# Performance work log

Hardware: AMD Instinct MI355X
Metric: run time of the kernel (lower is better)

Reference implementation:

```python
import jax, jax.numpy as jnp
import numpy as np

B, HGRID, D_MODEL = 4, 64, 96
D_INNER, D_STATE, DT_RANK, K = 192, 16, 6, 4
L = HGRID * HGRID


def setup_inputs() -> dict:
    key = jax.random.key(0)
    ks = jax.random.split(key, 12)
    C, N, R, D = D_INNER, D_STATE, DT_RANK, D_MODEL
    s = 0.02
    x = jax.random.normal(ks[0], (B, L, D), jnp.float32)
    in_proj_w = jax.random.normal(ks[1], (2 * C, D)) * s
    fft_w1 = jax.random.normal(ks[2], (C, C)) * s
    fft_b1 = jnp.zeros((C,))
    fft_w2 = jax.random.normal(ks[3], (C, C)) * s
    fft_b2 = jnp.zeros((C,))
    wave_w = jax.random.normal(ks[4], (C, C, 3, 3)) * s
    wave_b = jnp.zeros((C,))
    dw_w = jax.random.normal(ks[5], (C, 1, 3, 3)) * 0.1
    dw_b = jnp.zeros((C,))
    sym_w = jnp.asarray(0.3, jnp.float32)
    x_proj_w = jax.random.normal(ks[6], (K, R + 2 * N, C)) * s
    dt_std = R ** -0.5
    dt_w = jax.random.uniform(ks[7], (K, C, R), minval=-dt_std, maxval=dt_std)
    dt = jnp.exp(jax.random.uniform(ks[8], (K, C)) * (np.log(0.1) - np.log(0.001)) + np.log(0.001))
    dt = jnp.maximum(dt, 1e-4)
    dt_b = dt + jnp.log(-jnp.expm1(-dt))  # inverse softplus init as in dt_init
    A_logs = jnp.log(jnp.tile(jnp.arange(1, N + 1, dtype=jnp.float32), (K * C, 1)))  # [K*C, N]
    Ds = jnp.ones((K * C,))
    out_norm_g = jnp.ones((C,))
    out_norm_b = jnp.zeros((C,))
    out_proj_w = jax.random.normal(ks[9], (D, C)) * s
    rms_w = jnp.ones((D,))
    return dict(x=x, in_proj_w=in_proj_w, fft_w1=fft_w1, fft_b1=fft_b1, fft_w2=fft_w2,
                fft_b2=fft_b2, wave_w=wave_w, wave_b=wave_b, dw_w=dw_w, dw_b=dw_b,
                sym_w=sym_w, x_proj_w=x_proj_w, dt_w=dt_w, dt_b=dt_b, A_logs=A_logs,
                Ds=Ds, out_norm_g=out_norm_g, out_norm_b=out_norm_b,
                out_proj_w=out_proj_w, rms_w=rms_w)


def _conv2d(x, w, b, groups=1):
    y = jax.lax.conv_general_dilated(x, w, (1, 1), 'SAME', feature_group_count=groups,
                                     dimension_numbers=('NCHW', 'OIHW', 'NCHW'))
    return y + b[None, :, None, None]


def _haar_dwt(x):
    # orthonormal single-level Haar on 2x2 blocks
    a = x[..., 0::2, 0::2]; b = x[..., 0::2, 1::2]
    c = x[..., 1::2, 0::2]; d = x[..., 1::2, 1::2]
    return ((a + b + c + d) * 0.5, (a - b + c - d) * 0.5,
            (a + b - c - d) * 0.5, (a - b - c + d) * 0.5)


def _haar_idwt(ll, lh, hl, hh):
    a = (ll + lh + hl + hh) * 0.5; b = (ll - lh + hl - hh) * 0.5
    c = (ll + lh - hl - hh) * 0.5; d = (ll - lh - hl + hh) * 0.5
    Bb, Cc, H2, W2 = ll.shape
    top = jnp.stack([a, b], -1).reshape(Bb, Cc, H2, 2 * W2)
    bot = jnp.stack([c, d], -1).reshape(Bb, Cc, H2, 2 * W2)
    return jnp.stack([top, bot], -2).reshape(Bb, Cc, 2 * H2, 2 * W2)


def _freq_model(x, fft_w1, fft_b1, fft_w2, fft_b2, wave_w, wave_b):
    Bb, C, H, W = x.shape
    xf = jnp.fft.rfft2(x, norm='ortho')
    m = jax.nn.gelu(jnp.einsum('bchw,oc->bohw', jnp.abs(xf), fft_w1)
                    + fft_b1[None, :, None, None], approximate=False)
    mag = jnp.einsum('bchw,oc->bohw', m, fft_w2) + fft_b2[None, :, None, None]
    x_fourier = jnp.fft.irfft2(mag * jnp.exp(1j * jnp.angle(xf)), s=(H, W), norm='ortho')
    ll, lh, hl, hh = _haar_dwt(x)
    lh = _conv2d(lh, wave_w, wave_b)
    hl = _conv2d(hl, wave_w, wave_b)
    hh = _conv2d(hh, wave_w, wave_b)
    x_wavelet = _haar_idwt(ll, lh, hl, hh)
    return x + x_fourier + x_wavelet


def _selective_scan(xs, delta, A, Bs, Cs, Ds):
    # xs/delta: [B,K,C,L]; A: [K,C,N]; Bs/Cs: [B,K,N,L]; Ds: [K,C]
    Bb, Kk, C, Ll = xs.shape
    N = A.shape[-1]
    u_t = jnp.moveaxis(xs, -1, 0)     # [L,B,K,C]
    d_t = jnp.moveaxis(delta, -1, 0)
    B_t = jnp.moveaxis(Bs, -1, 0)     # [L,B,K,N]
    C_t = jnp.moveaxis(Cs, -1, 0)

    def step(h, inp):
        u, dd, bb, cc = inp
        h = jnp.exp(dd[..., None] * A) * h + (dd * u)[..., None] * bb[:, :, None, :]
        return h, jnp.einsum('bkcn,bkn->bkc', h, cc)

    h0 = jnp.zeros((Bb, Kk, C, N), xs.dtype)
    _, ys = jax.lax.scan(step, h0, (u_t, d_t, B_t, C_t))
    return jnp.moveaxis(ys, 0, -1) + xs * Ds[None, :, :, None]


def _forward(x, in_proj_w, fft_w1, fft_b1, fft_w2, fft_b2, wave_w, wave_b, dw_w, dw_b,
             sym_w, x_proj_w, dt_w, dt_b, A_logs, Ds, out_norm_g, out_norm_b,
             out_proj_w, rms_w):
    Bb, Ll, D = x.shape
    H = W = HGRID
    C, N, R = D_INNER, D_STATE, DT_RANK
    # RMSNorm (residual pre-norm)
    xn = x * jax.lax.rsqrt(jnp.mean(x * x, -1, keepdims=True) + 1e-5) * rms_w
    xz = xn.reshape(Bb, H, W, D) @ in_proj_w.T            # [B,H,W,2C]
    xi, z = jnp.split(xz, 2, axis=-1)
    xc = jnp.transpose(xi, (0, 3, 1, 2))                  # NCHW
    xc = xc + _freq_model(xc, fft_w1, fft_b1, fft_w2, fft_b2, wave_w, wave_b)
    a = jax.nn.silu(_conv2d(xc, dw_w, dw_b, groups=C))    # depthwise 3x3
    # 4-direction sequences
    x_flat = a.reshape(Bb, C, Ll)
    x_t = jnp.transpose(a, (0, 1, 3, 2)).reshape(Bb, C, Ll)
    xs = jnp.stack([x_flat, x_t, x_flat[..., ::-1], x_t[..., ::-1]], axis=1)  # [B,4,C,L]
    x_dbl = jnp.einsum('bkdl,kcd->bkcl', xs, x_proj_w)
    dts, Bs, Cs = jnp.split(x_dbl, [R, R + N], axis=2)
    dts = jnp.einsum('bkrl,kdr->bkdl', dts, dt_w)
    delta = jax.nn.softplus(dts + dt_b[None, :, :, None])
    A = -jnp.exp(A_logs).reshape(K, C, N)
    out_y = _selective_scan(xs, delta, A, Bs, Cs, Ds.reshape(K, C))  # [B,4,C,L]
    wh = jnp.transpose(out_y[:, 1].reshape(Bb, C, W, H), (0, 1, 3, 2)).reshape(Bb, C, Ll)
    iwh = jnp.transpose(out_y[:, 3, :, ::-1].reshape(Bb, C, W, H), (0, 1, 3, 2)).reshape(Bb, C, Ll)
    y = out_y[:, 0] + out_y[:, 2, :, ::-1] + wh + iwh     # [B,C,L]
    # lightweight symmetry enhancement
    y4 = y.reshape(Bb, C, H, W)
    wgt = jax.nn.sigmoid(sym_w)
    enh = y4 * (1 - wgt) + 0.5 * (y4 + y4[..., ::-1]) * wgt
    yf = y + 0.2 * enh.reshape(Bb, C, Ll)
    yf = jnp.transpose(yf, (0, 2, 1)).reshape(Bb, H, W, C)
    # LayerNorm
    mu = yf.mean(-1, keepdims=True)
    var = ((yf - mu) ** 2).mean(-1, keepdims=True)
    yn = (yf - mu) * jax.lax.rsqrt(var + 1e-5) * out_norm_g + out_norm_b
    out = (yn * jax.nn.silu(z)) @ out_proj_w.T
    return out.reshape(Bb, Ll, D) + x  # residual


def reference(x, in_proj_w, fft_w1, fft_b1, fft_w2, fft_b2, wave_w, wave_b, dw_w, dw_b,
              sym_w, x_proj_w, dt_w, dt_b, A_logs, Ds, out_norm_g, out_norm_b,
              out_proj_w, rms_w):
    return _forward(x, in_proj_w, fft_w1, fft_b1, fft_w2, fft_b2, wave_w, wave_b,
                    dw_w, dw_b, sym_w, x_proj_w, dt_w, dt_b, A_logs, Ds,
                    out_norm_g, out_norm_b, out_proj_w, rms_w)
```

## Files before the change

kernel.cpp:

```cpp
#include <hip/hip_runtime.h>
#include <hip/hip_bf16.h>

#define CI 192
#define LL_ 4096

typedef __bf16 v8bf __attribute__((ext_vector_type(8)));
typedef float  v4f  __attribute__((ext_vector_type(4)));
typedef float  v8f  __attribute__((ext_vector_type(8)));
typedef unsigned short v8us __attribute__((ext_vector_type(8)));

__device__ __forceinline__ unsigned short f2bf(float v){
  unsigned int u = __float_as_uint(v);
  return (unsigned short)((u + 0x7FFFu + ((u >> 16) & 1u)) >> 16);
}

__global__ __launch_bounds__(256) void k_zero(float* __restrict__ p, int n){
  int i = blockIdx.x*256 + threadIdx.x;
  if (i < n) p[i] = 0.f;
}

__global__ __launch_bounds__(256) void k_rms_inproj(const float* __restrict__ x,
    const float* __restrict__ rmsw, const float* __restrict__ ipw,
    float* __restrict__ xc, float* __restrict__ zT){
  int og = blockIdx.x & 7; int lt = (blockIdx.x >> 3) & 63; int b = blockIdx.x >> 9;
// ... 258 lines not shown
  __syncthreads();
  const unsigned short* base = lhT + (size_t)img*196608;
  for (int idx = tid; idx < 3072; idx += 256){
    int r = idx / 768; int t = idx - r*768;
    int pc = t / 24;   int icg = t - pc*24;
    int gr = 2*mt - 1 + r;
    if (gr >= 0 && gr < 32){
      v8us v = *(const v8us*)&base[((size_t)gr*32 + pc)*192 + icg*8];
      int pix = r*34 + 1 + pc;
      *(v8us*)&Aband[pix*192 + ((icg*8) ^ ((pix & 7) << 3))] = v;
    }
  }
  __syncthreads();
  v4f acc[4];
  #pragma unroll
  for (int t2 = 0; t2 < 4; t2++) acc[t2] = (v4f){0.f,0.f,0.f,0.f};
  #pragma unroll
  for (int q = 0; q < 9; q++){
    int ky = q/3, kx = q - ky*3;
    if (q < 8){
      #pragma unroll
      for (int icc = 0; icc < 6; icc++)
        bnxt[icc] = *(const v8us*)&wrow[(size_t)(q+1)*36864 + icc*32];
    }
    #pragma unroll
    for (int icc = 0; icc < 6; icc++){
      int c0 = icc*32;
      v8bf bv = __builtin_bit_cast(v8bf, bcur[icc]);
      #pragma unroll
      for (int t2 = 0; t2 < 4; t2++){
        int mm = t2*16 + n16;
        int pix = ((mm >> 5) + ky)*34 + (mm & 31) + kx;
        const unsigned short* Ap = &Aband[pix*192 + ((c0 + quad*8) ^ ((pix & 7) << 3))];
        v8bf av = __builtin_bit_cast(v8bf, *(const v8us*)Ap);
        acc[t2] = __builtin_amdgcn_mfma_f32_16x16x32_bf16(av, bv, acc[t2], 0, 0, 0);
      }
    }
    #pragma unroll
    for (int icc = 0; icc < 6; icc++) bcur[icc] = bnxt[icc];
  }
  __syncthreads();
  #pragma unroll
  for (int t2 = 0; t2 < 4; t2++)
    #pragma unroll
    for (int r = 0; r < 4; r++)
      T[(16*t2 + quad*4 + r)*65 + 16*wv + n16] = acc[t2][r];
  __syncthreads();
  float* outb = wnew + (size_t)img*196608;
  for (int idx = tid; idx < 4096; idx += 256){
    int mm = idx & 63, oc = idx >> 6;
    outb[(size_t)(o0 + oc)*1024 + mt*64 + mm] = T[mm*65 + oc];
  }
}

__global__ __launch_bounds__(256) void k_ifwd(const float* __restrict__ fre2,
    const float* __restrict__ fim2, const float* __restrict__ xc,
    const float* __restrict__ ll, const float* __restrict__ wnew, const float* __restrict__ wb,
    const float* __restrict__ dww, const float* __restrict__ dwb,
    float* __restrict__ ab, float* __restrict__ aT){
  int plane = blockIdx.x;
  int c = plane % 192;
  __shared__ __align__(16) float sm[13504];
  float* gr  = sm;
  float* gi  = sm + 2304;
  float* ur  = sm + 4608;
  float* ui  = sm + 6912;
  float* sx2 = sm + 9216;
  float* t64r = sm + 13376; float* t64i = sm + 13440;
  float* scratch = sm;
  int tid = threadIdx.x;
  {
    size_t gbase = (size_t)plane*2112;
    for (int idx = tid; idx < 528; idx += 256){
      float4 vr_ = *(const float4*)&fre2[gbase + 4*idx];
      float4 vi_ = *(const float4*)&fim2[gbase + 4*idx];
      #pragma unroll
      for (int e = 0; e < 4; e++){
        int i = 4*idx + e;
        int f = i/33, k = i - f*33;
        float re = (e==0)?vr_.x:((e==1)?vr_.y:((e==2)?vr_.z:vr_.w));
        float im = (e==0)?vi_.x:((e==1)?vi_.y:((e==2)?vi_.z:vi_.w));
        gr[f*36 + k] = re; gi[f*36 + k] = im;
      }
    }
  }
  if (tid < 64){ t64r[tid] = cospif((float)tid/32.0f); t64i[tid] = sinpif((float)tid/32.0f); }
  __syncthreads();
  {
    int hp = tid & 31, g = tid >> 5;
    float stepr = cospif((float)hp/32.0f), stepi = sinpif((float)hp/32.0f);
    v4f a0r = (v4f)0.f, a0i = (v4f)0.f, a1r = (v4f)0.f, a1i = (v4f)0.f;
    float b0r=0.f, b0i=0.f, b1r=0.f, b1i=0.f;
    for (int fb = 0; fb < 4; fb++){
      int m = ((fb*16)*hp) & 63;
      float twr = t64r[m], twi = t64i[m];
      for (int ff = 0; ff < 16; ff++){
        int f = fb*16 + ff;
        float sg = (f & 1) ? -1.f : 1.f;
        v4f Gr = *(const v4f*)&gr[f*36 + 4*g];
        v4f Gi = *(const v4f*)&gi[f*36 + 4*g];
        v4f pr = Gr*twr - Gi*twi;
        v4f pi = Gr*twi + Gi*twr;
        a0r += pr; a0i += pi;
        a1r += sg*pr; a1i += sg*pi;
        if (g == 0){
          float Tr = gr[f*36 + 32], Ti = gi[f*36 + 32];
          float prs = Tr*twr - Ti*twi, pis = Tr*twi + Ti*twr;
          b0r += prs; b0i += pis; b1r += sg*prs; b1i += sg*pis;
        }
        float nr = twr*stepr - twi*stepi, ni = twr*stepi + twi*stepr;
        twr = nr; twi = ni;
      }
    }
    #pragma unroll
    for (int j = 0; j < 4; j++){
      int k = 4*g + j;
      float ck = (k == 0) ? (1.f/64.f) : (2.f/64.f);
      ur[hp*36 + k] = a0r[j]*ck;       ui[hp*36 + k] = a0i[j]*ck;
      ur[(hp+32)*36 + k] = a1r[j]*ck;  ui[(hp+32)*36 + k] = a1i[j]*ck;
    }
    if (g == 0){
      ur[hp*36 + 32] = b0r*(1.f/64.f);      ui[hp*36 + 32] = b0i*(1.f/64.f);
      ur[(hp+32)*36 + 32] = b1r*(1.f/64.f); ui[(hp+32)*36 + 32] = b1i*(1.f/64.f);
    }
  }
  __syncthreads();
  {
    int h = tid & 63, wg = tid >> 6;
    v8f accL = (v8f)0.f, accH = (v8f)0.f, twr, twi, sr, si;
    #pragma unroll
    for (int j = 0; j < 8; j++){
      int wl = 8*wg + j;
      sr[j] = t64r[wl]; si[j] = t64i[wl];
      twr[j] = 1.f; twi[j] = 0.f;
    }
    float acc32 = 0.f;
    for (int kb = 0; kb < 8; kb++){
      v4f U4 = *(const v4f*)&ur[h*36 + 4*kb];
      v4f V4 = *(const v4f*)&ui[h*36 + 4*kb];
      #pragma unroll
      for (int e = 0; e < 4; e++){
        int k = 4*kb + e;
        float Ur = U4[e], Ui = V4[e];
        if (wg == 0) acc32 += (k & 1) ? -Ur : Ur;
        v8f p = Ur*twr, q = Ui*twi;
        accL += p - q;
        accH += p + q;
        v8f nr = twr*sr - twi*si;
        v8f ni = twr*si + twi*sr;
        twr = nr; twi = ni;
      }
    }
    {
      float Ur = ur[h*36 + 32], Ui = ui[h*36 + 32];
      if (wg == 0) acc32 += Ur;
      v8f p = Ur*twr, q = Ui*twi;
      accL += p - q;
      accH += p + q;
    }
    #pragma unroll
    for (int j = 0; j < 8; j++){
      int wl = 8*wg + j;
      sx2[h*65 + wl] = accL[j];
      if (wl == 0) sx2[h*65 + 32] = acc32;
      else         sx2[h*65 + 64 - wl] = accH[j];
    }
  }
  __syncthreads();
  {
    float bia = wb[c];
    #pragma unroll
    for (int it = 0; it < 8; it++){
      int idx = tid + it*256;
      int h = idx >> 5, pw = idx & 31;
      int w0 = pw*2;
      size_t q = (size_t)plane*1024 + (size_t)(h >> 1)*32 + pw;
      float LL = ll[q];
      float LH = wnew[q] + bia;
      float HL = wnew[786432 + q] + bia;
      float HH = wnew[1572864 + q] + bia;
      float2 xc2 = *(const float2*)&xc[(size_t)plane*4096 + h*64 + w0];
      float v0, v1;
      if (!(h & 1)){ v0 = (LL + LH + HL + HH)*0.5f; v1 = (LL - LH + HL - HH)*0.5f; }
      else         { v0 = (LL + LH - HL - HH)*0.5f; v1 = (LL - LH - HL + HH)*0.5f; }
      sx2[h*65 + w0]     += 2.0f*xc2.x + v0;
      sx2[h*65 + w0 + 1] += 2.0f*xc2.y + v1;
    }
  }
  __syncthreads();
  {
    float wk[9];
    #pragma unroll
    for (int q = 0; q < 9; q++) wk[q] = dww[c*9 + q];
    float dbv = dwb[c];
    int w = tid & 63, st = tid >> 6;
    int h0 = st*16;
    bool wl_ok = (w > 0), wr_ok = (w < 63);
    float r0l, r0c, r0r, r1l, r1c, r1r;
    if (h0 > 0){
      r0l = wl_ok ? sx2[(h0-1)*65 + w-1] : 0.f;
      r0c = sx2[(h0-1)*65 + w];
      r0r = wr_ok ? sx2[(h0-1)*65 + w+1] : 0.f;
    } else { r0l = 0.f; r0c = 0.f; r0r = 0.f; }
    r1l = wl_ok ? sx2[h0*65 + w-1] : 0.f;
    r1c = sx2[h0*65 + w];
    r1r = wr_ok ? sx2[h0*65 + w+1] : 0.f;
    #pragma unroll
    for (int hh2 = 0; hh2 < 16; hh2++){
      int h = h0 + hh2;
      float r2l, r2c, r2r;
      if (h < 63){
        r2l = wl_ok ? sx2[(h+1)*65 + w-1] : 0.f;
        r2c = sx2[(h+1)*65 + w];
        r2r = wr_ok ? sx2[(h+1)*65 + w+1] : 0.f;
      } else { r2l = 0.f; r2c = 0.f; r2r = 0.f; }
      float acc = dbv + r0l*wk[0] + r0c*wk[1] + r0r*wk[2]
                      + r1l*wk[3] + r1c*wk[4] + r1r*wk[5]
                      + r2l*wk[6] + r2c*wk[7] + r2r*wk[8];
      scratch[h*65 + w] = acc / (1.f + __expf(-acc));
      r0l = r1l; r0c = r1c; r0r = r1r;
      r1l = r2l; r1c = r2c; r1r = r2r;
    }
  }
  __syncthreads();
  float* abp = ab + (size_t)plane*4096;
  float* aTp = aT + (size_t)plane*4096;
  for (int p = tid; p < 4096; p += 256){
    abp[p] = scratch[(p >> 6)*65 + (p & 63)];
    aTp[p] = scratch[(p & 63)*65 + (p >> 6)];
  }
}

__global__ __launch_bounds__(256) void k_xproj(const float* __restrict__ ab,
    const float* __restrict__ aT, const float* __restrict__ xpw,
    float* __restrict__ Bsb, float* __restrict__ Csb, float* __restrict__ dlsb,
    float* __restrict__ xsb){
  int bid = blockIdx.x;
  int s = bid & 63; int k = (bid >> 6) & 3; int b = bid >> 8;
  int tid = threadIdx.x;
  __shared__ float als[96][65];
  __shared__ float dls[6][64];
  int l0 = s << 6;
  const float* src = (k & 1) ? aT : ab;
  bool rev = (k >= 2);
  int i = tid & 63, wg = tid >> 6;
  const float* wr[10];
  #pragma unroll
  for (int r = 0; r < 10; r++){
    int cp = wg + 4*r; if (cp > 37) cp = 37;
    int off = __builtin_amdgcn_readfirstlane((k*38 + cp)*192);
    wr[r] = xpw + off;
  }
  float acc[10];
  #pragma unroll
  for (int r = 0; r < 10; r++) acc[r] = 0.f;
  size_t xbase = ((size_t)(b*4 + k)*4096 + l0)*192;
  #pragma unroll
  for (int half = 0; half < 2; half++){
    int d0 = half*96;
    for (int idx = tid; idx < 1536; idx += 256){
      int d = idx >> 4, i4 = idx & 15;
      const float* rowp = src + ((size_t)b*192 + d0 + d)*4096;
      if (!rev){
        float4 v = *(const float4*)&rowp[l0 + 4*i4];
        als[d][4*i4+0] = v.x; als[d][4*i4+1] = v.y;
        als[d][4*i4+2] = v.z; als[d][4*i4+3] = v.w;
      } else {
        float4 v = *(const float4*)&rowp[4092 - l0 - 4*i4];
        als[d][4*i4+0] = v.w; als[d][4*i4+1] = v.z;
        als[d][4*i4+2] = v.y; als[d][4*i4+3] = v.x;
      }
    }
    __syncthreads();
    for (int d = 0; d < 96; d++){
      float v = als[d][i];
      #pragma unroll
      for (int r = 0; r < 10; r++) acc[r] += v*wr[r][d0 + d];
    }
    for (int idx = tid; idx < 1536; idx += 256){
      int ii = idx / 24, cc = (idx - (idx/24)*24)*4;
      float4 v;
      v.x = als[cc+0][ii]; v.y = als[cc+1][ii];
      v.z = als[cc+2][ii]; v.w = als[cc+3][ii];
      *(float4*)&xsb[xbase + (size_t)ii*192 + d0 + cc] = v;
    }
    __syncthreads();
  }
  #pragma unroll
  for (int r = 0; r < 10; r++){
    int cp = wg + 4*r;
    if (cp > 37) continue;
    if (cp < 6) dls[cp][i] = acc[r];
    else if (cp < 22) Bsb[((size_t)(b*4 + k)*16 + (cp - 6 ))*4096 + l0 + i] = acc[r];
    else              Csb[((size_t)(b*4 + k)*16 + (cp - 22))*4096 + l0 + i] = acc[r];
  }
  __syncthreads();
  size_t dbase = (size_t)((b*4 + k)*64 + s)*384;
  for (int j = tid; j < 384; j += 256){
    int ii = j/6, r = j - ii*6;
    dlsb[dbase + j] = dls[r][ii];
  }
}

__global__ __launch_bounds__(192) void k_scanA(const float* __restrict__ xsb,
    const float* __restrict__ dlsb, const float* __restrict__ Bsb,
    const float* __restrict__ dtw, const float* __restrict__ dtb,
    const float* __restrict__ alog, float* __restrict__ Pb, float* __restrict__ Qb){
  int bid = blockIdx.x; int s = bid & 63; int k = (bid >> 6) & 3; int b = bid >> 8;
  int c = threadIdx.x; int bk = b*4 + k;
  __shared__ float sdl[384];
  __shared__ float sB[16][64];
  size_t dbase = (size_t)(bk*64 + s)*384;
  for (int j = c; j < 384; j += 192) sdl[j] = dlsb[dbase + j];
  for (int j = c; j < 1024; j += 192){ int n = j >> 6, i = j & 63;
    sB[n][i] = Bsb[((size_t)bk*16 + n)*4096 + (s << 6) + i]; }
  __syncthreads();
  float A[16], P[16], Q[16];
  const float* arow = alog + ((size_t)k*192 + c)*16;
  bool fast = true;
  #pragma unroll
  for (int n = 0; n < 16; n++){
    A[n] = -__expf(arow[n]); P[n] = 1.f; Q[n] = 0.f;
    if (fabsf(A[n] + (float)(n+1)) > 1e-3f) fast = false;
  }
  float dw[6];
  #pragma unroll
  for (int r = 0; r < 6; r++) dw[r] = dtw[((size_t)k*192 + c)*6 + r];
  float db = dtb[k*192 + c];
  const float* xrow = xsb + ((size_t)bk*4096 + (s << 6))*192 + c;
  if (fast){
    for (int i = 0; i < 64; i++){
      float u = xrow[(size_t)i*192];
      float acc = db;
      #pragma unroll
      for (int r = 0; r < 6; r++) acc += sdl[i*6 + r]*dw[r];
      float ec = __expf(fminf(acc, 80.f));
      float dl = __logf(1.f + ec);
      float e1 = __builtin_amdgcn_rcpf(1.f + ec);
      float du = dl*u;
      float e = 1.f;
      #pragma unroll
      for (int n = 0; n < 16; n++){
        e *= e1;
        P[n] *= e;
        Q[n] = Q[n]*e + du*sB[n][i];
      }
    }
  } else {
    for (int i = 0; i < 64; i++){
      float u = xrow[(size_t)i*192];
      float acc = db;
      #pragma unroll
      for (int r = 0; r < 6; r++) acc += sdl[i*6 + r]*dw[r];
      float ec = __expf(fminf(acc, 80.f));
      float dl = __logf(1.f + ec);
      float du = dl*u;
      #pragma unroll
      for (int n = 0; n < 16; n++){
        float e = __expf(dl*A[n]);
        P[n] *= e;
        Q[n] = Q[n]*e + du*sB[n][i];
      }
    }
  }
  size_t pbase = ((size_t)(bk*64 + s)*16)*192 + c;
  #pragma unroll
  for (int n = 0; n < 16; n++){ Pb[pbase + (size_t)n*192] = P[n]; Qb[pbase + (size_t)n*192] = Q[n]; }
}

__global__ __launch_bounds__(256) void k_scanB(float* __restrict__ Pb,
    const float* __restrict__ Qb){
  int id = blockIdx.x*256 + threadIdx.x;
  int c = id % 192; int rest = id / 192; int n = rest % 16; int bk = rest / 16;
  float h = 0.f;
  for (int s = 0; s < 64; s++){
    size_t o = (((size_t)bk*64 + s)*16 + n)*192 + c;
    float P = Pb[o], Q = Qb[o];
    Pb[o] = h;
    h = P*h + Q;
  }
}

__global__ __launch_bounds__(192) void k_scanC_buf(const float* __restrict__ xsb,
    const float* __restrict__ dlsb, const float* __restrict__ Bsb, const float* __restrict__ Csb,
    const float* __restrict__ hinb, const float* __restrict__ dtw, const float* __restrict__ dtb,
    const float* __restrict__ alog, const float* __restrict__ Dsp, float* __restrict__ Y){
  int bid = blockIdx.x; int s = bid & 63; int k = (bid >> 6) & 3; int b = bid >> 8;
  int c = threadIdx.x; int bk = b*4 + k;
  __shared__ float sdl[384];
  __shared__ float sB[16][64];
  __shared__ float sC[16][64];
  size_t dbase = (size_t)(bk*64 + s)*384;
  for (int j = c; j < 384; j += 192) sdl[j] = dlsb[dbase + j];
  for (int j = c; j < 1024; j += 192){ int n = j >> 6, i = j & 63;
    size_t o = ((size_t)bk*16 + n)*4096 + (s << 6) + i;
    sB[n][i] = Bsb[o]; sC[n][i] = Csb[o]; }
  __syncthreads();
  float A[16], h[16];
  const float* arow = alog + ((size_t)k*192 + c)*16;
  bool fast = true;
  #pragma unroll
  for (int n = 0; n < 16; n++){
    A[n] = -__expf(arow[n]);
    if (fabsf(A[n] + (float)(n+1)) > 1e-3f) fast = false;
  }
  size_t hbase = ((size_t)(bk*64 + s)*16)*192 + c;
  #pragma unroll
  for (int n = 0; n < 16; n++) h[n] = hinb[hbase + (size_t)n*192];
  float dw[6];
  #pragma unroll
  for (int r = 0; r < 6; r++) dw[r] = dtw[((size_t)k*192 + c)*6 + r];
  float db = dtb[k*192 + c];
  float Dc = Dsp[k*192 + c];
  const float* xrow = xsb + ((size_t)bk*4096 + (s << 6))*192 + c;
  float* Yk = Y + (((size_t)bk*4096 + (s << 6))*192) + c;
  if (fast){
    for (int i = 0; i < 64; i++){
      float u = xrow[(size_t)i*192];
      float acc = db;
      #pragma unroll
      for (int r = 0; r < 6; r++) acc += sdl[i*6 + r]*dw[r];
      float ec = __expf(fminf(acc, 80.f));
      float dl = __logf(1.f + ec);
      float e1 = __builtin_amdgcn_rcpf(1.f + ec);
      float du = dl*u;
      float e = 1.f;
      float y = 0.f;
      #pragma unroll
      for (int n = 0; n < 16; n++){
        e *= e1;
        h[n] = h[n]*e + du*sB[n][i];
        y += h[n]*sC[n][i];
      }
      Yk[(size_t)i*192] = y + u*Dc;
    }
  } else {
    for (int i = 0; i < 64; i++){
      float u = xrow[(size_t)i*192];
      float acc = db;
      #pragma unroll
      for (int r = 0; r < 6; r++) acc += sdl[i*6 + r]*dw[r];
      float ec = __expf(fminf(acc, 80.f));
      float dl = __logf(1.f + ec);
      float du = dl*u;
      float y = 0.f;
      #pragma unroll
      for (int n = 0; n < 16; n++){
        float e = __expf(dl*A[n]);
        h[n] = h[n]*e + du*sB[n][i];
        y += h[n]*sC[n][i];
      }
      Yk[(size_t)i*192] = y + u*Dc;
    }
  }
}

__global__ __launch_bounds__(192) void k_scanC_atom(const float* __restrict__ xsb,
    const float* __restrict__ dlsb, const float* __restrict__ Bsb, const float* __restrict__ Csb,
    const float* __restrict__ hinb, const float* __restrict__ dtw, const float* __restrict__ dtb,
    const float* __restrict__ alog, const float* __restrict__ Dsp, float* __restrict__ yb){
  int bid = blockIdx.x; int s = bid & 63; int k = (bid >> 6) & 3; int b = bid >> 8;
  int c = threadIdx.x; int bk = b*4 + k;
  __shared__ float sdl[384];
  __shared__ float sB[16][64];
  __shared__ float sC[16][64];
  size_t dbase = (size_t)(bk*64 + s)*384;
  for (int j = c; j < 384; j += 192) sdl[j] = dlsb[dbase + j];
  for (int j = c; j < 1024; j += 192){ int n = j >> 6, i = j & 63;
    size_t o = ((size_t)bk*16 + n)*4096 + (s << 6) + i;
    sB[n][i] = Bsb[o]; sC[n][i] = Csb[o]; }
  __syncthreads();
  float A[16], h[16];
  const float* arow = alog + ((size_t)k*192 + c)*16;
  bool fast = true;
  #pragma unroll
  for (int n = 0; n < 16; n++){
    A[n] = -__expf(arow[n]);
    if (fabsf(A[n] + (float)(n+1)) > 1e-3f) fast = false;
  }
  size_t hbase = ((size_t)(bk*64 + s)*16)*192 + c;
  #pragma unroll
  for (int n = 0; n < 16; n++) h[n] = hinb[hbase + (size_t)n*192];
  float dw[6];
  #pragma unroll
  for (int r = 0; r < 6; r++) dw[r] = dtw[((size_t)k*192 + c)*6 + r];
  float db = dtb[k*192 + c];
  float Dc = Dsp[k*192 + c];
  const float* xrow = xsb + ((size_t)bk*4096 + (s << 6))*192 + c;
  int p0, pst;
  if (k == 0){ p0 = s << 6;        pst = 1;  }
  else if (k == 1){ p0 = s;        pst = 64; }
  else if (k == 2){ p0 = 4095 - (s << 6); pst = -1; }
  else { p0 = 4095 - s;            pst = -64; }
  for (int i = 0; i < 64; i++){
    float u = xrow[(size_t)i*192];
    float acc = db;
    #pragma unroll
    for (int r = 0; r < 6; r++) acc += sdl[i*6 + r]*dw[r];
    float ec = __expf(fminf(acc, 80.f));
    float dl = __logf(1.f + ec);
    float du = dl*u;
    float y = 0.f;
    if (fast){
      float e1 = __builtin_amdgcn_rcpf(1.f + ec);
      float e = 1.f;
      #pragma unroll
      for (int n = 0; n < 16; n++){
        e *= e1;
        h[n] = h[n]*e + du*sB[n][i];
        y += h[n]*sC[n][i];
      }
    } else {
      #pragma unroll
      for (int n = 0; n < 16; n++){
        float e = __expf(dl*A[n]);
        h[n] = h[n]*e + du*sB[n][i];
        y += h[n]*sC[n][i];
      }
    }
    y += u*Dc;
    atomicAdd(&yb[((size_t)b*4096 + p0 + pst*i)*192 + c], y);
  }
}

__global__ __launch_bounds__(256) void k_enh(const float* __restrict__ yb,
    const float* __restrict__ symw, float* __restrict__ yfb){
  int id = blockIdx.x*256 + threadIdx.x;
  int c = id % 192; int rest = id / 192; int l = rest & 4095; int b = rest >> 12;
  int w = l & 63; int lr = (l | 63) - w;
  float v  = yb[id];
  float vr = yb[(((size_t)b << 12) + lr)*192 + c];
  float wg = 1.f/(1.f + __expf(-symw[0]));
  float enh = v*(1.f - wg) + 0.5f*(v + vr)*wg;
  yfb[id] = v + 0.2f*enh;
}

__global__ __launch_bounds__(256) void k_final_comb(const float* __restrict__ Y,
    const float* __restrict__ symw, const float* __restrict__ zT,
    const float* __restrict__ g, const float* __restrict__ bta,
    const float* __restrict__ opw, const float* __restrict__ x, float* __restrict__ out){
  int og = blockIdx.x & 1; int lt = (blockIdx.x >> 1) & 127; int b = blockIdx.x >> 8;
  int h = lt >> 1, wsel = lt & 1;
  __shared__ float sv[32][193];
  __shared__ float wt[192*48];
  __shared__ float sg[192], sb2[192];
  __shared__ float smu[32], srs[32];
  __shared__ int lmap[32];
  int tid = threadIdx.x;
  const size_t S = (size_t)4096*192;
  float wg = 1.f/(1.f + __expf(-symw[0]));
  if (tid < 32){
    int r = tid;
    int w = (r < 16) ? (wsel*16 + r) : (63 - wsel*16 - (r - 16));
    lmap[r] = h*64 + w;
  }
  for (int idx = tid; idx < 1536; idx += 256){
    int r = idx / 48, c4 = (idx - (idx/48)*48)*4;
    int w = (r < 16) ? (wsel*16 + r) : (63 - wsel*16 - (r - 16));
    int l = h*64 + w;
    int p1 = (w << 6) | h;
    size_t base = (size_t)(b*4)*S + c4;
    float4 v0 = *(const float4*)&Y[base + (size_t)l*192];
    float4 v1 = *(const float4*)&Y[base + S + (size_t)p1*192];
    float4 v2 = *(const float4*)&Y[base + 2*S + (size_t)(4095 - l)*192];
    float4 v3 = *(const float4*)&Y[base + 3*S + (size_t)(4095 - p1)*192];
    sv[r][c4+0] = v0.x + v1.x + v2.x + v3.x;
    sv[r][c4+1] = v0.y + v1.y + v2.y + v3.y;
    sv[r][c4+2] = v0.z + v1.z + v2.z + v3.z;
    sv[r][c4+3] = v0.w + v1.w + v2.w + v3.w;
  }
  if (tid < 192){ sg[tid] = g[tid]; sb2[tid] = bta[tid]; }
  int o0 = og*48;
  for (int idx = tid; idx < 9216; idx += 256){ int o = idx % 48, c = idx/48;
    wt[c*48 + o] = opw[(size_t)(o0 + o)*192 + c]; }
  __syncthreads();
  float yreg[24];
  #pragma unroll
  for (int t = 0; t < 24; t++){
    int idx = tid + t*256;
    int r = idx / 192, cc = idx - r*192;
    int rp = (r < 16) ? r + 16 : r - 16;
    float v = sv[r][cc], vp = sv[rp][cc];
    float enh = v*(1.f - wg) + 0.5f*(v + vp)*wg;
    yreg[t] = v + 0.2f*enh;
  }
  __syncthreads();
  #pragma unroll
  for (int t = 0; t < 24; t++){
    int idx = tid + t*256;
    int r = idx / 192, cc = idx - r*192;
    sv[r][cc] = yreg[t];
  }
  __syncthreads();
  if (tid < 32){
    float s1 = 0.f, s2 = 0.f;
    for (int c = 0; c < 192; c++){ float v = sv[tid][c]; s1 += v; s2 += v*v; }
    float mu = s1*(1.0f/192.0f);
    smu[tid] = mu; srs[tid] = rsqrtf(s2*(1.0f/192.0f) - mu*mu + 1e-5f);
  }
  __syncthreads();
  for (int idx = tid; idx < 6144; idx += 256){ int l = idx & 31, c = idx >> 5;
    float zv = zT[((size_t)b*192 + c)*4096 + lmap[l]];
    float v = sv[l][c];
    float yn = (v - smu[l])*srs[l]*sg[c] + sb2[c];
    sv[l][c] = yn * (zv/(1.f + __expf(-zv)));
  }
  __syncthreads();
  int l = tid & 31, grp = tid >> 5;
  float acc[6];
  #pragma unroll
  for (int j = 0; j < 6; j++) acc[j] = 0.f;
  for (int c = 0; c < 192; c++){
    float svv = sv[l][c];
    const float* wr = &wt[c*48 + grp*6];
    #pragma unroll
    for (int j = 0; j < 6; j += 2){
      float2 w2 = *(const float2*)&wr[j];
      acc[j]   += svv*w2.x; acc[j+1] += svv*w2.y;
    }
  }
  size_t ob = ((size_t)b*4096 + lmap[l])*96 + o0 + grp*6;
  #pragma unroll
  for (int j = 0; j < 6; j++) acc[j] += x[ob + j];
  #pragma unroll
  for (int j = 0; j < 6; j += 2){
    float2 v2; v2.x = acc[j]; v2.y = acc[j+1];
    *(float2*)&out[ob + j] = v2;
  }
}

__global__ __launch_bounds__(256) void k_final(const float* __restrict__ yf,
    const float* __restrict__ zT, const float* __restrict__ g, const float* __restrict__ bta,
    const float* __restrict__ opw, const float* __restrict__ x, float* __restrict__ out){
  int og = blockIdx.x & 1; int lt = (blockIdx.x >> 1) & 127; int b = blockIdx.x >> 8;
  int l0 = lt << 5;
  __shared__ float sv[32][193];
  __shared__ float wt[192*48];
  __shared__ float sg[192], sb2[192];
  __shared__ float smu[32], srs[32];
  int tid = threadIdx.x;
  for (int idx = tid; idx < 6144; idx += 256){ int r = idx/192, c = idx - r*192;
    sv[r][c] = yf[((size_t)b*4096 + l0 + r)*192 + c]; }
  if (tid < 192){ sg[tid] = g[tid]; sb2[tid] = bta[tid]; }
  int o0 = og*48;
  for (int idx = tid; idx < 9216; idx += 256){ int o = idx % 48, c = idx/48;
    wt[c*48 + o] = opw[(size_t)(o0 + o)*192 + c]; }
  __syncthreads();
  if (tid < 32){
    float s1 = 0.f, s2 = 0.f;
    for (int c = 0; c < 192; c++){ float v = sv[tid][c]; s1 += v; s2 += v*v; }
    float mu = s1*(1.0f/192.0f);
    smu[tid] = mu; srs[tid] = rsqrtf(s2*(1.0f/192.0f) - mu*mu + 1e-5f);
  }
  __syncthreads();
  for (int idx = tid; idx < 6144; idx += 256){ int l = idx & 31, c = idx >> 5;
    float zv = zT[((size_t)b*192 + c)*4096 + l0 + l];
    float v = sv[l][c];
    float yn = (v - smu[l])*srs[l]*sg[c] + sb2[c];
    sv[l][c] = yn * (zv/(1.f + __expf(-zv)));
  }
  __syncthreads();
  int l = tid & 31, grp = tid >> 5;
  float acc[6];
  #pragma unroll
  for (int j = 0; j < 6; j++) acc[j] = 0.f;
  for (int c = 0; c < 192; c++){
    float svv = sv[l][c];
    const float* wr = &wt[c*48 + grp*6];
    #pragma unroll
    for (int j = 0; j < 6; j += 2){
      float2 w2 = *(const float2*)&wr[j];
      acc[j]   += svv*w2.x; acc[j+1] += svv*w2.y;
    }
  }
  size_t ob = ((size_t)b*4096 + l0 + l)*96 + o0 + grp*6;
  #pragma unroll
  for (int j = 0; j < 6; j++) acc[j] += x[ob + j];
  #pragma unroll
  for (int j = 0; j < 6; j += 2){
    float2 v2; v2.x = acc[j]; v2.y = acc[j+1];
    *(float2*)&out[ob + j] = v2;
  }
}

extern "C" void kernel_launch(void* const* d_in, const int* in_sizes, int n_in,
                              void* d_out, int out_size, void* d_ws, size_t ws_size,
                              hipStream_t stream){
  (void)in_sizes; (void)n_in; (void)out_size;
  const float* ix   = (const float*)d_in[0];
  const float* ipw  = (const float*)d_in[1];
  const float* fw1  = (const float*)d_in[2];
  const float* fb1  = (const float*)d_in[3];
  const float* fw2  = (const float*)d_in[4];
  const float* fb2  = (const float*)d_in[5];
  const float* ww   = (const float*)d_in[6];
  const float* wb   = (const float*)d_in[7];
  const float* dww  = (const float*)d_in[8];
  const float* dwb  = (const float*)d_in[9];
  const float* symw = (const float*)d_in[10];
  const float* xpw  = (const float*)d_in[11];
  const float* dtw  = (const float*)d_in[12];
  const float* dtb  = (const float*)d_in[13];
  const float* alog = (const float*)d_in[14];
  const float* Dsp  = (const float*)d_in[15];
  const float* ong  = (const float*)d_in[16];
  const float* onb  = (const float*)d_in[17];
  const float* opw  = (const float*)d_in[18];
  const float* rmsw = (const float*)d_in[19];

  float* W = (float*)d_ws;
  const size_t SZ_BLC = 3145728, SZ_F = 1622016, SZ_H = 786432;
  float* zT  = W;
  float* ab  = zT + SZ_BLC;
  float* R0  = ab + SZ_BLC;
  float* xc    = R0;
  float* fre   = xc  + SZ_BLC;
  float* fim   = fre + SZ_F;
  float* fab   = fim + SZ_F;
  float* mb    = fab + SZ_F;
  float* llb   = mb  + SZ_F;
  float* lhb   = llb + SZ_H;
  float* wnew  = lhb + 3*SZ_H;
  unsigned short* wqb2 = (unsigned short*)(wnew + 2359296);
  unsigned short* lhT  = wqb2 + 331776;
  float* Bsb  = R0;
  float* Csb  = Bsb + 1048576;
  float* dlsb = Csb + 1048576;
  float* xsb  = dlsb + 393216;
  float* Pb   = xsb + 12582912;
  float* aT   = Pb;
  float* Qb   = Pb + SZ_BLC;
  float* Yb   = Qb;
  float* ybA  = Qb + SZ_BLC;
  float* yfb  = xsb;

  const size_t NEED_BIG = (size_t)(6291456 + 30801920) * 4;
  bool bigws = (ws_size >= NEED_BIG);

  hipLaunchKernelGGL(k_rms_inproj, dim3(2048),   dim3(256), 0, stream, ix, rmsw, ipw, xc, zT);
  hipLaunchKernelGGL(k_dft_fwd,    dim3(4*192),  dim3(256), 0, stream, xc, fre, fim, fab,
                     llb, lhb, lhb + SZ_H, lhb + 2*SZ_H);
  hipLaunchKernelGGL(k_cvt_w,      dim3(1296),   dim3(256), 0, stream, ww, wqb2);
  hipLaunchKernelGGL(k_prep_lhT,   dim3(1152),   dim3(256), 0, stream, lhb, lhT);
  hipLaunchKernelGGL(k_cmix1,      dim3(864),    dim3(256), 0, stream, fab, fw1, fb1, mb);
  hipLaunchKernelGGL(k_cmix2,      dim3(864),    dim3(256), 0, stream, mb, fw2, fb2, fre, fim, fab);
  hipLaunchKernelGGL(k_wconv_mfma, dim3(576),    dim3(256), 0, stream, lhT, wqb2, wnew);
  hipLaunchKernelGGL(k_ifwd,       dim3(768),    dim3(256), 0, stream, fre, fim, xc, llb, wnew, wb, dww, dwb, ab, aT);
  hipLaunchKernelGGL(k_xproj,      dim3(1024),   dim3(256), 0, stream, ab, aT, xpw, Bsb, Csb, dlsb, xsb);
  hipLaunchKernelGGL(k_scanA,      dim3(1024),   dim3(192), 0, stream, xsb, dlsb, Bsb, dtw, dtb, alog, Pb, Qb);
  hipLaunchKernelGGL(k_scanB,      dim3(192),    dim3(256), 0, stream, Pb, Qb);
  if (bigws){
    hipLaunchKernelGGL(k_scanC_buf,  dim3(1024), dim3(192), 0, stream, xsb, dlsb, Bsb, Csb, Pb, dtw, dtb, alog, Dsp, Yb);
    hipLaunchKernelGGL(k_final_comb, dim3(1024), dim3(256), 0, stream, Yb, symw, zT, ong, onb, opw, ix, (float*)d_out);
  } else {
    hipLaunchKernelGGL(k_zero,       dim3(12288), dim3(256), 0, stream, ybA, (int)SZ_BLC);
    hipLaunchKernelGGL(k_scanC_atom, dim3(1024),  dim3(192), 0, stream, xsb, dlsb, Bsb, Csb, Pb, dtw, dtb, alog, Dsp, ybA);
    hipLaunchKernelGGL(k_enh,        dim3(12288), dim3(256), 0, stream, ybA, symw, yfb);
    hipLaunchKernelGGL(k_final,      dim3(1024),  dim3(256), 0, stream, yfb, zT, ong, onb, opw, ix, (float*)d_out);
  }
}
```

Measured before the change: 536.0 us.

## Split scan state dimension across thread pairs and shrink final-combine row tiles

The chunked selective-scan kernels (scanA and scanC_buf) now use 384 threads per block, so each channel's 16 state elements are split between two threads. The upper-half thread precomputes e1^8 so the fast exponential chain stays correct, and scanC merges the two partial outputs with a lane shuffle. k_final_comb now processes 16 rows per block instead of 32 and launches twice as many blocks. Both changes aim to raise parallelism and occupancy, at the cost of redundant dt/softplus work per channel and reloading the output-projection weights more often.

```diff
diff --git a/kernel.cpp b/kernel.cpp
--- a/kernel.cpp
+++ b/kernel.cpp
@@ -584,27 +584,33 @@
   }
 }
 
-__global__ __launch_bounds__(192) void k_scanA(const float* __restrict__ xsb,
+__global__ __launch_bounds__(384) void k_scanA(const float* __restrict__ xsb,
     const float* __restrict__ dlsb, const float* __restrict__ Bsb,
     const float* __restrict__ dtw, const float* __restrict__ dtb,
     const float* __restrict__ alog, float* __restrict__ Pb, float* __restrict__ Qb){
   int bid = blockIdx.x; int s = bid & 63; int k = (bid >> 6) & 3; int b = bid >> 8;
-  int c = threadIdx.x; int bk = b*4 + k;
+  int tid = threadIdx.x;
+  int c = tid >> 1, half = tid & 1;
+  int bk = b*4 + k;
   __shared__ float sdl[384];
   __shared__ float sB[16][64];
   size_t dbase = (size_t)(bk*64 + s)*384;
-  for (int j = c; j < 384; j += 192) sdl[j] = dlsb[dbase + j];
-  for (int j = c; j < 1024; j += 192){ int n = j >> 6, i = j & 63;
+  for (int j = tid; j < 384; j += 384) sdl[j] = dlsb[dbase + j];
+  for (int j = tid; j < 1024; j += 384){ int n = j >> 6, i = j & 63;
     sB[n][i] = Bsb[((size_t)bk*16 + n)*4096 + (s << 6) + i]; }
   __syncthreads();
-  float A[16], P[16], Q[16];
+  int n0 = half*8;
+  float A[8], P[8], Q[8];
   const float* arow = alog + ((size_t)k*192 + c)*16;
   bool fast = true;
   #pragma unroll
   for (int n = 0; n < 16; n++){
-    A[n] = -__expf(arow[n]); P[n] = 1.f; Q[n] = 0.f;
-    if (fabsf(A[n] + (float)(n+1)) > 1e-3f) fast = false;
-  }
+    float a = -__expf(arow[n]);
+    if (fabsf(a + (float)(n+1)) > 1e-3f) fast = false;
+    if (n >= n0 && n < n0 + 8) A[n - n0] = a;
+  }
+  #pragma unroll
+  for (int n = 0; n < 8; n++){ P[n] = 1.f; Q[n] = 0.f; }
   float dw[6];
   #pragma unroll
   for (int r = 0; r < 6; r++) dw[r] = dtw[((size_t)k*192 + c)*6 + r];
@@ -621,11 +627,12 @@
       float e1 = __builtin_amdgcn_rcpf(1.f + ec);
       float du = dl*u;
       float e = 1.f;
-      #pragma unroll
-      for (int n = 0; n < 16; n++){
+      if (half){ float e2 = e1*e1; float e4 = e2*e2; e = e4*e4; }
+      #pragma unroll
+      for (int n = 0; n < 8; n++){
         e *= e1;
         P[n] *= e;
-        Q[n] = Q[n]*e + du*sB[n][i];
+        Q[n] = Q[n]*e + du*sB[n0+n][i];
       }
     }
   } else {
@@ -638,16 +645,19 @@
       float dl = __logf(1.f + ec);
       float du = dl*u;
       #pragma unroll
-      for (int n = 0; n < 16; n++){
+      for (int n = 0; n < 8; n++){
         float e = __expf(dl*A[n]);
         P[n] *= e;
-        Q[n] = Q[n]*e + du*sB[n][i];
+        Q[n] = Q[n]*e + du*sB[n0+n][i];
       }
     }
   }
   size_t pbase = ((size_t)(bk*64 + s)*16)*192 + c;
   #pragma unroll
-  for (int n = 0; n < 16; n++){ Pb[pbase + (size_t)n*192] = P[n]; Qb[pbase + (size_t)n*192] = Q[n]; }
+  for (int n = 0; n < 8; n++){
+    Pb[pbase + (size_t)(n0+n)*192] = P[n];
+    Qb[pbase + (size_t)(n0+n)*192] = Q[n];
+  }
 }
 
 __global__ __launch_bounds__(256) void k_scanB(float* __restrict__ Pb,
@@ -663,32 +673,36 @@
   }
 }
 
-__global__ __launch_bounds__(192) void k_scanC_buf(const float* __restrict__ xsb,
+__global__ __launch_bounds__(384) void k_scanC_buf(const float* __restrict__ xsb,
     const float* __restrict__ dlsb, const float* __restrict__ Bsb, const float* __restrict__ Csb,
     const float* __restrict__ hinb, const float* __restrict__ dtw, const float* __restrict__ dtb,
     const float* __restrict__ alog, const float* __restrict__ Dsp, float* __restrict__ Y){
   int bid = blockIdx.x; int s = bid & 63; int k = (bid >> 6) & 3; int b = bid >> 8;
-  int c = threadIdx.x; int bk = b*4 + k;
+  int tid = threadIdx.x;
+  int c = tid >> 1, half = tid & 1;
+  int bk = b*4 + k;
   __shared__ float sdl[384];
   __shared__ float sB[16][64];
   __shared__ float sC[16][64];
   size_t dbase = (size_t)(bk*64 + s)*384;
-  for (int j = c; j < 384; j += 192) sdl[j] = dlsb[dbase + j];
-  for (int j = c; j < 1024; j += 192){ int n = j >> 6, i = j & 63;
+  for (int j = tid; j < 384; j += 384) sdl[j] = dlsb[dbase + j];
+  for (int j = tid; j < 1024; j += 384){ int n = j >> 6, i = j & 63;
     size_t o = ((size_t)bk*16 + n)*4096 + (s << 6) + i;
     sB[n][i] = Bsb[o]; sC[n][i] = Csb[o]; }
   __syncthreads();
-  float A[16], h[16];
+  int n0 = half*8;
+  float A[8], h[8];
   const float* arow = alog + ((size_t)k*192 + c)*16;
   bool fast = true;
   #pragma unroll
   for (int n = 0; n < 16; n++){
-    A[n] = -__expf(arow[n]);
-    if (fabsf(A[n] + (float)(n+1)) > 1e-3f) fast = false;
+    float a = -__expf(arow[n]);
+    if (fabsf(a + (float)(n+1)) > 1e-3f) fast = false;
+    if (n >= n0 && n < n0 + 8) A[n - n0] = a;
   }
   size_t hbase = ((size_t)(bk*64 + s)*16)*192 + c;
   #pragma unroll
-  for (int n = 0; n < 16; n++) h[n] = hinb[hbase + (size_t)n*192];
+  for (int n = 0; n < 8; n++) h[n] = hinb[hbase + (size_t)(n0+n)*192];
   float dw[6];
   #pragma unroll
   for (int r = 0; r < 6; r++) dw[r] = dtw[((size_t)k*192 + c)*6 + r];
@@ -707,14 +721,16 @@
       float e1 = __builtin_amdgcn_rcpf(1.f + ec);
       float du = dl*u;
       float e = 1.f;
+      if (half){ float e2 = e1*e1; float e4 = e2*e2; e = e4*e4; }
       float y = 0.f;
       #pragma unroll
-      for (int n = 0; n < 16; n++){
+      for (int n = 0; n < 8; n++){
         e *= e1;
-        h[n] = h[n]*e + du*sB[n][i];
-        y += h[n]*sC[n][i];
-      }
-      Yk[(size_t)i*192] = y + u*Dc;
+        h[n] = h[n]*e + du*sB[n0+n][i];
+        y += h[n]*sC[n0+n][i];
+      }
+      float yo = y + __shfl_xor(y, 1);
+      if (half == 0) Yk[(size_t)i*192] = yo + u*Dc;
     }
   } else {
     for (int i = 0; i < 64; i++){
@@ -727,12 +743,13 @@
       float du = dl*u;
       float y = 0.f;
       #pragma unroll
-      for (int n = 0; n < 16; n++){
+      for (int n = 0; n < 8; n++){
         float e = __expf(dl*A[n]);
-        h[n] = h[n]*e + du*sB[n][i];
-        y += h[n]*sC[n][i];
-      }
-      Yk[(size_t)i*192] = y + u*Dc;
+        h[n] = h[n]*e + du*sB[n0+n][i];
+        y += h[n]*sC[n0+n][i];
+      }
+      float yo = y + __shfl_xor(y, 1);
+      if (half == 0) Yk[(size_t)i*192] = yo + u*Dc;
     }
   }
 }
@@ -821,24 +838,25 @@
     const float* __restrict__ symw, const float* __restrict__ zT,
     const float* __restrict__ g, const float* __restrict__ bta,
     const float* __restrict__ opw, const float* __restrict__ x, float* __restrict__ out){
-  int og = blockIdx.x & 1; int lt = (blockIdx.x >> 1) & 127; int b = blockIdx.x >> 8;
-  int h = lt >> 1, wsel = lt & 1;
-  __shared__ float sv[32][193];
+  int rt = blockIdx.x & 511; int b = blockIdx.x >> 9;
+  int og = rt & 1; int tile = rt >> 1;
+  int h = tile >> 2, wsel = tile & 3;
+  __shared__ float sv[16][193];
   __shared__ float wt[192*48];
   __shared__ float sg[192], sb2[192];
-  __shared__ float smu[32], srs[32];
-  __shared__ int lmap[32];
+  __shared__ float smu[16], srs[16];
+  __shared__ int lmap[16];
   int tid = threadIdx.x;
   const size_t S = (size_t)4096*192;
   float wg = 1.f/(1.f + __expf(-symw[0]));
-  if (tid < 32){
+  if (tid < 16){
     int r = tid;
-    int w = (r < 16) ? (wsel*16 + r) : (63 - wsel*16 - (r - 16));
+    int w = (r < 8) ? (wsel*8 + r) : (63 - wsel*8 - (r - 8));
     lmap[r] = h*64 + w;
   }
-  for (int idx = tid; idx < 1536; idx += 256){
+  for (int idx = tid; idx < 768; idx += 256){
     int r = idx / 48, c4 = (idx - (idx/48)*48)*4;
-    int w = (r < 16) ? (wsel*16 + r) : (63 - wsel*16 - (r - 16));
+    int w = (r < 8) ? (wsel*8 + r) : (63 - wsel*8 - (r - 8));
     int l = h*64 + w;
     int p1 = (w << 6) | h;
     size_t base = (size_t)(b*4)*S + c4;
@@ -856,59 +874,50 @@
   for (int idx = tid; idx < 9216; idx += 256){ int o = idx % 48, c = idx/48;
     wt[c*48 + o] = opw[(size_t)(o0 + o)*192 + c]; }
   __syncthreads();
-  float yreg[24];
-  #pragma unroll
-  for (int t = 0; t < 24; t++){
+  float yreg[12];
+  #pragma unroll
+  for (int t = 0; t < 12; t++){
     int idx = tid + t*256;
     int r = idx / 192, cc = idx - r*192;
-    int rp = (r < 16) ? r + 16 : r - 16;
+    int rp = (r < 8) ? r + 8 : r - 8;
     float v = sv[r][cc], vp = sv[rp][cc];
     float enh = v*(1.f - wg) + 0.5f*(v + vp)*wg;
     yreg[t] = v + 0.2f*enh;
   }
   __syncthreads();
   #pragma unroll
-  for (int t = 0; t < 24; t++){
+  for (int t = 0; t < 12; t++){
     int idx = tid + t*256;
     int r = idx / 192, cc = idx - r*192;
     sv[r][cc] = yreg[t];
   }
   __syncthreads();
-  if (tid < 32){
+  if (tid < 16){
     float s1 = 0.f, s2 = 0.f;
     for (int c = 0; c < 192; c++){ float v = sv[tid][c]; s1 += v; s2 += v*v; }
     float mu = s1*(1.0f/192.0f);
     smu[tid] = mu; srs[tid] = rsqrtf(s2*(1.0f/192.0f) - mu*mu + 1e-5f);
   }
   __syncthreads();
-  for (int idx = tid; idx < 6144; idx += 256){ int l = idx & 31, c = idx >> 5;
+  for (int idx = tid; idx < 3072; idx += 256){ int l = idx & 15, c = idx >> 4;
     float zv = zT[((size_t)b*192 + c)*4096 + lmap[l]];
     float v = sv[l][c];
     float yn = (v - smu[l])*srs[l]*sg[c] + sb2[c];
     sv[l][c] = yn * (zv/(1.f + __expf(-zv)));
   }
   __syncthreads();
-  int l = tid & 31, grp = tid >> 5;
-  float acc[6];
-  #pragma unroll
-  for (int j = 0; j < 6; j++) acc[j] = 0.f;
+  int l = tid & 15, grp = tid >> 4;
+  float acc[3];
+  #pragma unroll
+  for (int j = 0; j < 3; j++) acc[j] = 0.f;
   for (int c = 0; c < 192; c++){
     float svv = sv[l][c];
-    const float* wr = &wt[c*48 + grp*6];
-    #pragma unroll
-    for (int j = 0; j < 6; j += 2){
-      float2 w2 = *(const float2*)&wr[j];
-      acc[j]   += svv*w2.x; acc[j+1] += svv*w2.y;
-    }
-  }
-  size_t ob = ((size_t)b*4096 + lmap[l])*96 + o0 + grp*6;
-  #pragma unroll
-  for (int j = 0; j < 6; j++) acc[j] += x[ob + j];
-  #pragma unroll
-  for (int j = 0; j < 6; j += 2){
-    float2 v2; v2.x = acc[j]; v2.y = acc[j+1];
-    *(float2*)&out[ob + j] = v2;
-  }
+    const float* wr = &wt[c*48 + grp*3];
+    acc[0] += svv*wr[0]; acc[1] += svv*wr[1]; acc[2] += svv*wr[2];
+  }
+  size_t ob = ((size_t)b*4096 + lmap[l])*96 + o0 + grp*3;
+  #pragma unroll
+  for (int j = 0; j < 3; j++) out[ob + j] = acc[j] + x[ob + j];
 }
 
 __global__ __launch_bounds__(256) void k_final(const float* __restrict__ yf,
@@ -1029,11 +1038,11 @@
   hipLaunchKernelGGL(k_wconv_mfma, dim3(576),    dim3(256), 0, stream, lhT, wqb2, wnew);
   hipLaunchKernelGGL(k_ifwd,       dim3(768),    dim3(256), 0, stream, fre, fim, xc, llb, wnew, wb, dww, dwb, ab, aT);
   hipLaunchKernelGGL(k_xproj,      dim3(1024),   dim3(256), 0, stream, ab, aT, xpw, Bsb, Csb, dlsb, xsb);
-  hipLaunchKernelGGL(k_scanA,      dim3(1024),   dim3(192), 0, stream, xsb, dlsb, Bsb, dtw, dtb, alog, Pb, Qb);
+  hipLaunchKernelGGL(k_scanA,      dim3(1024),   dim3(384), 0, stream, xsb, dlsb, Bsb, dtw, dtb, alog, Pb, Qb);
   hipLaunchKernelGGL(k_scanB,      dim3(192),    dim3(256), 0, stream, Pb, Qb);
   if (bigws){
-    hipLaunchKernelGGL(k_scanC_buf,  dim3(1024), dim3(192), 0, stream, xsb, dlsb, Bsb, Csb, Pb, dtw, dtb, alog, Dsp, Yb);
-    hipLaunchKernelGGL(k_final_comb, dim3(1024), dim3(256), 0, stream, Yb, symw, zT, ong, onb, opw, ix, (float*)d_out);
+    hipLaunchKernelGGL(k_scanC_buf,  dim3(1024), dim3(384), 0, stream, xsb, dlsb, Bsb, Csb, Pb, dtw, dtb, alog, Dsp, Yb);
+    hipLaunchKernelGGL(k_final_comb, dim3(2048), dim3(256), 0, stream, Yb, symw, zT, ong, onb, opw, ix, (float*)d_out);
   } else {
     hipLaunchKernelGGL(k_zero,       dim3(12288), dim3(256), 0, stream, ybA, (int)SZ_BLC);
     hipLaunchKernelGGL(k_scanC_atom, dim3(1024),  dim3(192), 0, stream, xsb, dlsb, Bsb, Csb, Pb, dtw, dtb, alog, Dsp, ybA);
```

Measured after the change: 583.8 us. +8.9%, slower.
